# Kernel optimization log

Measured on AMD Instinct MI355X. Metric: run time of the kernel, lower is better.

## Reference

```python
import jax, jax.numpy as jnp
import numpy as np

B, Z, H, D, T, L = 2048, 64, 256, 8, 250, 2


def setup_inputs() -> dict:
    key = jax.random.key(0)
    ks = jax.random.split(key, 10)
    s = 0.05  # small init scale for stable LSTM dynamics
    n = lambda k, shp, sc=1.0: jax.random.normal(k, shp, dtype=jnp.float32) * sc
    return {
        "z": n(ks[0], (B, Z)),
        "target_seq": n(ks[1], (B, T, D)),
        "fc_hidden_w": n(ks[2], (Z, H * L), s),
        "fc_hidden_b": jnp.zeros((H * L,), jnp.float32),
        "fc_cell_w": n(ks[3], (Z, H * L), s),
        "fc_cell_b": jnp.zeros((H * L,), jnp.float32),
        "W_ih0": n(ks[4], (D, 4 * H), s),
        "W_hh0": n(ks[5], (H, 4 * H), s),
        "b_ih0": jnp.zeros((4 * H,), jnp.float32),
        "b_hh0": jnp.zeros((4 * H,), jnp.float32),
        "W_ih1": n(ks[6], (H, 4 * H), s),
        "W_hh1": n(ks[7], (H, 4 * H), s),
        "b_ih1": jnp.zeros((4 * H,), jnp.float32),
        "b_hh1": jnp.zeros((4 * H,), jnp.float32),
        "fc_out_w": n(ks[8], (H, D), s),
        "fc_out_b": jnp.zeros((D,), jnp.float32),
    }


def _lstm_cell(x, h, c, Wih, Whh, bih, bhh):
    # PyTorch gate order: i, f, g, o
    gates = x @ Wih + bih + h @ Whh + bhh  # [B, 4H]
    i, f, g, o = jnp.split(gates, 4, axis=-1)
    c_new = jax.nn.sigmoid(f) * c + jax.nn.sigmoid(i) * jnp.tanh(g)
    h_new = jax.nn.sigmoid(o) * jnp.tanh(c_new)
    return h_new, c_new


def reference(z, target_seq, fc_hidden_w, fc_hidden_b, fc_cell_w, fc_cell_b,
              W_ih0, W_hh0, b_ih0, b_hh0, W_ih1, W_hh1, b_ih1, b_hh1,
              fc_out_w, fc_out_b):
    bsz = z.shape[0]
    # Faithful to torch .view(num_layers, batch, hidden) on [B, H*L] output
    h0_all = (z @ fc_hidden_w + fc_hidden_b).reshape(L, bsz, H)
    c0_all = (z @ fc_cell_w + fc_cell_b).reshape(L, bsz, H)
    # Teacher forcing ratio 1.0: input at step t is target[:, t-1] (zeros at t=0)
    first = jnp.zeros((bsz, 1, target_seq.shape[-1]), target_seq.dtype)
    inputs = jnp.concatenate([first, target_seq[:, :-1]], axis=1)  # [B, T, D]
    xs = jnp.transpose(inputs, (1, 0, 2))  # time-major [T, B, D]

    def step(carry, xt):
        h0, c0, h1, c1 = carry
        h0, c0 = _lstm_cell(xt, h0, c0, W_ih0, W_hh0, b_ih0, b_hh0)
        h1, c1 = _lstm_cell(h0, h1, c1, W_ih1, W_hh1, b_ih1, b_hh1)
        return (h0, c0, h1, c1), h1

    init = (h0_all[0], c0_all[0], h0_all[1], c0_all[1])
    _, hs = jax.lax.scan(step, init, xs)  # hs: [T, B, H]
    hs = jnp.transpose(hs, (1, 0, 2))  # [B, T, H]
    reconstructed = hs @ fc_out_w + fc_out_b  # [B, T, D]
    return reconstructed
```

## Files before the change

### kernel.cpp

```cpp
#include <hip/hip_runtime.h>
#include <cstddef>
#include <cstdint>


#define BSZ    2048
#define ZDIM   64
#define HDIM   256
#define DDIM   8
#define TSTEPS 250
#define ROWS   16
#define NWG    (BSZ / ROWS)
#define NTH    512
#define G4     1024
#define WSTR   264

typedef __attribute__((ext_vector_type(4))) int v4i;

__device__ __forceinline__ unsigned short f2bf(float x) {
  union { float f; unsigned u; } v; v.f = x;
  unsigned r = v.u + 0x7fff + ((v.u >> 16) & 1);
  return (unsigned short)(r >> 16);
}
__device__ __forceinline__ float bf2f(unsigned short b) {
  union { unsigned u; float f; } v; v.u = (unsigned)b << 16; return v.f;
}
__device__ __forceinline__ float fexp2(float x) { return __builtin_amdgcn_exp2f(x); }
__device__ __forceinline__ float frcp(float x)  { return __builtin_amdgcn_rcpf(x); }
__device__ __forceinline__ float sigm(float x)  { return frcp(1.f + fexp2(-1.44269504f * x)); }
__device__ __forceinline__ float tanh_(float x) { return 2.f * frcp(1.f + fexp2(-2.88539008f * x)) - 1.f; }
__device__ __forceinline__ char q8(float x, float s) {
  float v = fminf(fmaxf(x * s, -127.f), 127.f);
  return (char)(int)__builtin_rintf(v);
}
__device__ __forceinline__ void q8pair(float h, float s, char* hi, char* lo) {
  float hs = fminf(fmaxf(h * s, -127.f), 127.f);
  float hq = __builtin_rintf(hs);
  *hi = (char)(int)hq;
  *lo = (char)(int)__builtin_rintf((hs - hq) * 254.f);
}

__global__ void init_state(const float* __restrict__ z,
                           const float* __restrict__ Wfh, const float* __restrict__ bfh,
                           const float* __restrict__ Wfc, const float* __restrict__ bfc,
                           char* __restrict__ h0h, char* __restrict__ h0l,
                           char* __restrict__ h1h, char* __restrict__ h1l,
                           float* __restrict__ c0s, float* __restrict__ c1s)
{
  int idx = blockIdx.x * 256 + threadIdx.x;
  int b = idx >> 8;
  int j = idx & 255;
  int col = ((b & 1) << 8) | j;
  const float* z0 = z + (size_t)(b >> 1) * ZDIM;
  const float* z1 = z + (size_t)(1024 + (b >> 1)) * ZDIM;
  float h0 = bfh[col], c0v = bfc[col], h1 = bfh[col], c1v = bfc[col];
  for (int k = 0; k < ZDIM; ++k) {
    float wh = Wfh[k * 512 + col];
    float wc = Wfc[k * 512 + col];
    float a = z0[k], bb = z1[k];
    h0  += a * wh;  c0v += a * wc;
    h1  += bb * wh; c1v += bb * wc;
  }
  char hi, lo;
  q8pair(h0, 31.75f, &hi, &lo); h0h[idx] = hi; h0l[idx] = lo;
  q8pair(h1, 31.75f, &hi, &lo); h1h[idx] = hi; h1l[idx] = lo;
  c0s[idx] = c0v; c1s[idx] = c1v;
}

__global__ void col_scales(const float* __restrict__ Whh0,
                           const float* __restrict__ Wih1, const float* __restrict__ Whh1,
                           float* __restrict__ cs0, float* __restrict__ qs0,
                           float* __restrict__ cs1, float* __restrict__ qs1)
{
  int c = blockIdx.x * 256 + threadIdx.x;
  if (c < 1024) {
    float m = 0.f;
    for (int k = 0; k < 256; ++k) m = fmaxf(m, fabsf(Whh0[(size_t)k * G4 + c]));
    cs0[c] = m * (1.f / 16129.f);
    qs0[c] = 127.f / m;
  } else {
    c -= 1024;
    float m = 0.f;
    for (int k = 0; k < 256; ++k) m = fmaxf(m, fabsf(Whh1[(size_t)k * G4 + c]));
    for (int k = 0; k < 256; ++k) m = fmaxf(m, fabsf(Wih1[(size_t)k * G4 + c]));
    cs1[c] = m * (1.f / 16129.f);
    qs1[c] = 127.f / m;
  }
}

__global__ void pack_i8(const float* __restrict__ Whh0,
                        const float* __restrict__ Wih1, const float* __restrict__ Whh1,
                        const float* __restrict__ qs0, const float* __restrict__ qs1,
                        char* __restrict__ p0, char* __restrict__ p1)
{
  int tt   = blockIdx.x * 4 + (threadIdx.x >> 6);
  int lane = threadIdx.x & 63;
  int l15 = lane & 15, lq = lane >> 4;
  union { char c[16]; uint4 u; } v;
  if (tt < 256) {
    int w = tt >> 5, kc = (tt >> 3) & 3, i = tt & 7;
    int nt = (i >> 1) * 16 + 2 * w + (i & 1);
    int col = nt * 16 + l15;
    float q = qs0[col];
    for (int j = 0; j < 16; ++j) {
      int k = kc * 64 + lq * 16 + j;
      v.c[j] = q8(Whh0[(size_t)k * G4 + col], q);
    }
    *(uint4*)(p0 + (size_t)tt * 1024 + lane * 16) = v.u;
  } else {
    int t1 = tt - 256;
    int w = t1 >> 6, kc = (t1 >> 3) & 7, i = t1 & 7;
    int nt = (i >> 1) * 16 + 2 * w + (i & 1);
    int col = nt * 16 + l15;
    float q = qs1[col];
    for (int j = 0; j < 16; ++j) {
      int k = kc * 64 + lq * 16 + j;
      float wv = (k < 256) ? Whh1[(size_t)k * G4 + col]
                           : Wih1[(size_t)(k - 256) * G4 + col];
      v.c[j] = q8(wv, q);
    }
    *(uint4*)(p1 + (size_t)t1 * 1024 + lane * 16) = v.u;
  }
}

__global__ __launch_bounds__(NTH, 1) void lstm_run(
    const float* __restrict__ target,
    const char* __restrict__ p0, const char* __restrict__ p1,
    const float* __restrict__ bih0, const float* __restrict__ bhh0,
    const float* __restrict__ bih1, const float* __restrict__ bhh1,
    const float* __restrict__ Wih0,
    const float* __restrict__ Wout, const float* __restrict__ bout,
    const char* __restrict__ h0h, const char* __restrict__ h0l,
    const char* __restrict__ h1h, const char* __restrict__ h1l,
    const float* __restrict__ c0s, const float* __restrict__ c1s,
    const float* __restrict__ cs0, const float* __restrict__ cs1,
    float* __restrict__ out)
{
  __shared__ uint4 X4h[1024];
  __shared__ uint4 X4l[1024];
  __shared__ unsigned short h1f[2][16 * WSTR];
  __shared__ unsigned short woutT[8 * WSTR];

  const int tid  = threadIdx.x;
  const int w    = tid >> 6;
  const int lane = tid & 63;
  const int l15  = lane & 15;
  const int lq   = lane >> 4;
  const int b0   = blockIdx.x * ROWS;
  char* Xch = (char*)X4h;
  char* Xcl = (char*)X4l;

  {
    int m = tid & 15, blk = tid >> 4;
    const char* sh = (blk < 16) ? h1h : h0h;
    const char* sl = (blk < 16) ? h1l : h0l;
    int jblk = blk & 15;
    X4h[blk * 16 + m] = *(const uint4*)(sh + (size_t)(b0 + m) * HDIM + jblk * 16);
    X4l[blk * 16 + m] = *(const uint4*)(sl + (size_t)(b0 + m) * HDIM + jblk * 16);
  }
  for (int i = tid; i < HDIM * DDIM; i += NTH) {
    int k = i >> 3, d = i & 7;
    woutT[d * WSTR + k] = f2bf(Wout[i]);
  }

  const int myrow = lq * 4;
  const int jc0   = 32 * w + l15;
  float c0r[2][4], c1r[2][4];
  float bA0[8], bA1[8], csA0[8], csA1[8];
  float wx[8][8];
#pragma unroll
  for (int i = 0; i < 8; ++i) {
    int col = (i >> 1) * 256 + jc0 + 16 * (i & 1);
    bA0[i]  = bih0[col] + bhh0[col];
    bA1[i]  = bih1[col] + bhh1[col];
    csA0[i] = cs0[col];
    csA1[i] = cs1[col];
#pragma unroll
    for (int d = 0; d < 8; ++d) wx[i][d] = Wih0[d * G4 + col];
  }
#pragma unroll
  for (int cc = 0; cc < 2; ++cc) {
    int j = jc0 + cc * 16;
#pragma unroll
    for (int r = 0; r < 4; ++r) {
      c0r[cc][r] = c0s[(size_t)(b0 + myrow + r) * HDIM + j];
      c1r[cc][r] = c1s[(size_t)(b0 + myrow + r) * HDIM + j];
    }
  }
  const int opr = tid >> 5, opd = (tid >> 2) & 7, opq = tid & 3;
  const float bo_out = bout[opd];

  const char* gp0 = p0 + (size_t)w * 32768 + lane * 16;
  const char* gp1 = p1 + (size_t)w * 65536 + lane * 16;

  v4i breg[8];
#pragma unroll
  for (int s = 0; s < 8; ++s)
    breg[s] = *(const v4i*)(gp0 + (size_t)s * 1024);

  __syncthreads();

#pragma unroll 1
  for (int t = 0; t < TSTEPS; ++t) {
    const int xc = (t & 1) << 9;
    const int xn = xc ^ 512;

    float4 xa[4], xb[4];
    if (t > 0) {
      const float* xp = target + (size_t)(b0 + myrow) * (TSTEPS * DDIM)
                               + (size_t)(t - 1) * DDIM;
#pragma unroll
      for (int r = 0; r < 4; ++r) {
        xa[r] = *(const float4*)(xp + (size_t)r * (TSTEPS * DDIM));
        xb[r] = *(const float4*)(xp + (size_t)r * (TSTEPS * DDIM) + 4);
      }
    } else {
#pragma unroll
      for (int r = 0; r < 4; ++r) {
        xa[r] = make_float4(0.f, 0.f, 0.f, 0.f);
        xb[r] = make_float4(0.f, 0.f, 0.f, 0.f);
      }
    }

    const float sc0 = (t <= 1) ? 4.f : 1.f;
    const float sc1 = (t == 0) ? 4.f : 1.f;
    const float wq0 = (t == 0) ? 31.75f : 127.f;

    v4i acch[8], accl[8];
    const v4i zi = {0, 0, 0, 0};

#pragma unroll
    for (int i = 0; i < 8; ++i) { acch[i] = zi; accl[i] = zi; }
    {
      v4i ah, al;
#pragma unroll 8
      for (int j = 0; j < 32; ++j) {
        const int i = j & 7;
        if (i == 0) {
          int kc = j >> 3;
          int aidx = xc + (16 + kc * 4 + lq) * 16 + l15;
          ah = __builtin_bit_cast(v4i, X4h[aidx]);
          al = __builtin_bit_cast(v4i, X4l[aidx]);
        }
        acch[i] = __builtin_amdgcn_mfma_i32_16x16x64_i8(ah, breg[i], acch[i], 0, 0, 0);
        accl[i] = __builtin_amdgcn_mfma_i32_16x16x64_i8(al, breg[i], accl[i], 0, 0, 0);
        const int jn = j + 8;
        breg[i] = (jn < 32) ? *(const v4i*)(gp0 + (size_t)jn * 1024)
                            : *(const v4i*)(gp1 + (size_t)(jn - 32) * 1024);
      }
    }

    if (t > 0) {
      const unsigned short* hf = h1f[(t & 1) ^ 1];
      float s_ = 0.f;
#pragma unroll
      for (int i = 0; i < 16; ++i) {
        ushort4 hx = *(const ushort4*)&hf[opr * WSTR + i * 16 + opq * 4];
        ushort4 wv = *(const ushort4*)&woutT[opd * WSTR + i * 16 + opq * 4];
        s_ += bf2f(hx.x) * bf2f(wv.x) + bf2f(hx.y) * bf2f(wv.y)
            + bf2f(hx.z) * bf2f(wv.z) + bf2f(hx.w) * bf2f(wv.w);
      }
      s_ += __shfl_xor(s_, 1);
      s_ += __shfl_xor(s_, 2);
      if (opq == 0)
        out[(size_t)(b0 + opr) * (TSTEPS * DDIM) + (size_t)(t - 1) * DDIM + opd] =
            s_ + bo_out;
    }

    {
#pragma unroll
      for (int cc = 0; cc < 2; ++cc) {
        float gf4[4][4];
#pragma unroll
        for (int g = 0; g < 4; ++g) {
          int i = g * 2 + cc;
          float cs = csA0[i] * sc0;
#pragma unroll
          for (int r = 0; r < 4; ++r)
            gf4[g][r] = ((float)acch[i][r] + (float)accl[i][r] * (1.f / 254.f)) * cs + bA0[i];
        }
#pragma unroll
        for (int g = 0; g < 4; ++g) {
          int i = g * 2 + cc;
#pragma unroll
          for (int r = 0; r < 4; ++r)
            gf4[g][r] += xa[r].x * wx[i][0] + xa[r].y * wx[i][1]
                       + xa[r].z * wx[i][2] + xa[r].w * wx[i][3]
                       + xb[r].x * wx[i][4] + xb[r].y * wx[i][5]
                       + xb[r].z * wx[i][6] + xb[r].w * wx[i][7];
        }
#pragma unroll
        for (int r = 0; r < 4; ++r) {
          float iv = sigm(gf4[0][r]);
          float fv = sigm(gf4[1][r]);
          float gv = tanh_(gf4[2][r]);
          float ov = sigm(gf4[3][r]);
          c0r[cc][r] = fv * c0r[cc][r] + iv * gv;
          char hi, lo;
          q8pair(ov * tanh_(c0r[cc][r]), wq0, &hi, &lo);
          int off = (xn + (16 + 2 * w + cc) * 16 + myrow + r) * 16 + l15;
          Xch[off] = hi; Xcl[off] = lo;
        }
      }
    }
    __syncthreads();

#pragma unroll
    for (int i = 0; i < 8; ++i) { acch[i] = zi; accl[i] = zi; }
    {
      v4i ah, al;
#pragma unroll 8
      for (int j = 0; j < 64; ++j) {
        const int i = j & 7;
        if (i == 0) {
          int kc = j >> 3;
          int aidx = (kc < 4) ? (xc + (kc * 4 + lq) * 16 + l15)
                              : (xn + (16 + (kc - 4) * 4 + lq) * 16 + l15);
          ah = __builtin_bit_cast(v4i, X4h[aidx]);
          al = __builtin_bit_cast(v4i, X4l[aidx]);
        }
        acch[i] = __builtin_amdgcn_mfma_i32_16x16x64_i8(ah, breg[i], acch[i], 0, 0, 0);
        accl[i] = __builtin_amdgcn_mfma_i32_16x16x64_i8(al, breg[i], accl[i], 0, 0, 0);
        const int jn = j + 8;
        breg[i] = (jn < 64) ? *(const v4i*)(gp1 + (size_t)jn * 1024)
                            : *(const v4i*)(gp0 + (size_t)(jn - 64) * 1024);
      }
    }

#pragma unroll
    for (int cc = 0; cc < 2; ++cc)
#pragma unroll
      for (int r = 0; r < 4; ++r) {
        float di = ((float)acch[0 + cc][r] + (float)accl[0 + cc][r] * (1.f / 254.f));
        float df = ((float)acch[2 + cc][r] + (float)accl[2 + cc][r] * (1.f / 254.f));
        float dg = ((float)acch[4 + cc][r] + (float)accl[4 + cc][r] * (1.f / 254.f));
        float dv = ((float)acch[6 + cc][r] + (float)accl[6 + cc][r] * (1.f / 254.f));
        float iv = sigm(di * csA1[0 + cc] * sc1 + bA1[0 + cc]);
        float fv = sigm(df * csA1[2 + cc] * sc1 + bA1[2 + cc]);
        float gv = tanh_(dg * csA1[4 + cc] * sc1 + bA1[4 + cc]);
        float ov = sigm(dv * csA1[6 + cc] * sc1 + bA1[6 + cc]);
        c1r[cc][r] = fv * c1r[cc][r] + iv * gv;
        float h = ov * tanh_(c1r[cc][r]);
        char hi, lo;
        q8pair(h, 127.f, &hi, &lo);
        int off = (xn + (2 * w + cc) * 16 + myrow + r) * 16 + l15;
        Xch[off] = hi; Xcl[off] = lo;
        h1f[t & 1][(myrow + r) * WSTR + jc0 + cc * 16] = f2bf(h);
      }
    __syncthreads();
  }

  {
    const unsigned short* hf = h1f[(TSTEPS - 1) & 1];
    float s_ = 0.f;
#pragma unroll
    for (int i = 0; i < 16; ++i) {
      ushort4 hx = *(const ushort4*)&hf[opr * WSTR + i * 16 + opq * 4];
      ushort4 wv = *(const ushort4*)&woutT[opd * WSTR + i * 16 + opq * 4];
      s_ += bf2f(hx.x) * bf2f(wv.x) + bf2f(hx.y) * bf2f(wv.y)
          + bf2f(hx.z) * bf2f(wv.z) + bf2f(hx.w) * bf2f(wv.w);
    }
    s_ += __shfl_xor(s_, 1);
    s_ += __shfl_xor(s_, 2);
    if (opq == 0)
      out[(size_t)(b0 + opr) * (TSTEPS * DDIM) + (size_t)(TSTEPS - 1) * DDIM + opd] =
          s_ + bo_out;
  }
}

extern "C" void kernel_launch(void* const* d_in, const int* in_sizes, int n_in,
                              void* d_out, int out_size, void* d_ws, size_t ws_size,
                              hipStream_t stream) {
  const float* z    = (const float*)d_in[0];
  const float* tgt  = (const float*)d_in[1];
  const float* Wfh  = (const float*)d_in[2];
  const float* bfh  = (const float*)d_in[3];
  const float* Wfc  = (const float*)d_in[4];
  const float* bfc  = (const float*)d_in[5];
  const float* Wih0 = (const float*)d_in[6];
  const float* Whh0 = (const float*)d_in[7];
  const float* bih0 = (const float*)d_in[8];
  const float* bhh0 = (const float*)d_in[9];
  const float* Wih1 = (const float*)d_in[10];
  const float* Whh1 = (const float*)d_in[11];
  const float* bih1 = (const float*)d_in[12];
  const float* bhh1 = (const float*)d_in[13];
  const float* Wout = (const float*)d_in[14];
  const float* bout = (const float*)d_in[15];

  char* ws = (char*)d_ws;
  char*  p0   = ws;
  char*  p1   = ws + 262144;
  char*  h0h  = ws + 786432;
  char*  h0l  = ws + 1310720;
  char*  h1h  = ws + 1835008;
  char*  h1l  = ws + 2359296;
  float* c0s  = (float*)(ws + 2883584);
  float* c1s  = (float*)(ws + 4980736);
  float* cs0  = (float*)(ws + 7077888);
  float* qs0  = (float*)(ws + 7081984);
  float* cs1  = (float*)(ws + 7086080);
  float* qs1  = (float*)(ws + 7090176);

  hipLaunchKernelGGL(init_state, dim3(BSZ * HDIM / 256), dim3(256), 0, stream,
                     z, Wfh, bfh, Wfc, bfc, h0h, h0l, h1h, h1l, c0s, c1s);
  hipLaunchKernelGGL(col_scales, dim3(8), dim3(256), 0, stream,
                     Whh0, Wih1, Whh1, cs0, qs0, cs1, qs1);
  hipLaunchKernelGGL(pack_i8, dim3(192), dim3(256), 0, stream,
                     Whh0, Wih1, Whh1, qs0, qs1, p0, p1);
  hipLaunchKernelGGL(lstm_run, dim3(NWG), dim3(NTH), 0, stream,
                     tgt, p0, p1, bih0, bhh0, bih1, bhh1, Wih0, Wout, bout,
                     h0h, h0l, h1h, h1l, c0s, c1s, cs0, cs1, (float*)d_out);
}
```

Measured before the change: 3.076 ms.

## Double threads per block: each wave owns one 16-column gate slice

Raises the LSTM kernel from 8 to 16 waves per workgroup, with each wave handling one 16-column hidden slice across all four gates instead of two. Weight packing is reordered to match, halving the MFMA count and streamed int8 weight tiles per wave per step. The input-projection weights move from registers into LDS to cut register pressure, and the output projection is spread over 1024 threads. This trades more waves per barrier and extra LDS traffic for more parallelism hiding MFMA and global-load latency in the serial time loop.

```diff
diff --git a/kernel.cpp b/kernel.cpp
--- a/kernel.cpp
+++ b/kernel.cpp
@@ -10,7 +10,7 @@
 #define TSTEPS 250
 #define ROWS   16
 #define NWG    (BSZ / ROWS)
-#define NTH    512
+#define NTH    1024
 #define G4     1024
 #define WSTR   264
 
@@ -97,9 +97,9 @@
   int l15 = lane & 15, lq = lane >> 4;
   union { char c[16]; uint4 u; } v;
   if (tt < 256) {
-    int w = tt >> 5, kc = (tt >> 3) & 3, i = tt & 7;
-    int nt = (i >> 1) * 16 + 2 * w + (i & 1);
-    int col = nt * 16 + l15;
+    int w = tt >> 4, r = tt & 15;
+    int kc = r >> 2, g = r & 3;
+    int col = g * 256 + w * 16 + l15;
     float q = qs0[col];
     for (int j = 0; j < 16; ++j) {
       int k = kc * 64 + lq * 16 + j;
@@ -108,9 +108,9 @@
     *(uint4*)(p0 + (size_t)tt * 1024 + lane * 16) = v.u;
   } else {
     int t1 = tt - 256;
-    int w = t1 >> 6, kc = (t1 >> 3) & 7, i = t1 & 7;
-    int nt = (i >> 1) * 16 + 2 * w + (i & 1);
-    int col = nt * 16 + l15;
+    int w = t1 >> 5, r = t1 & 31;
+    int kc = r >> 2, g = r & 3;
+    int col = g * 256 + w * 16 + l15;
     float q = qs1[col];
     for (int j = 0; j < 16; ++j) {
       int k = kc * 64 + lq * 16 + j;
@@ -122,7 +122,7 @@
   }
 }
 
-__global__ __launch_bounds__(NTH, 1) void lstm_run(
+__global__ __launch_bounds__(NTH, 4) void lstm_run(
     const float* __restrict__ target,
     const char* __restrict__ p0, const char* __restrict__ p1,
     const float* __restrict__ bih0, const float* __restrict__ bhh0,
@@ -139,7 +139,7 @@
   __shared__ uint4 X4l[1024];
   __shared__ unsigned short h1f[2][16 * WSTR];
   __shared__ unsigned short woutT[8 * WSTR];
-
+  __shared__ float wxl[1024 * 8];
   const int tid  = threadIdx.x;
   const int w    = tid >> 6;
   const int lane = tid & 63;
@@ -149,7 +149,7 @@
   char* Xch = (char*)X4h;
   char* Xcl = (char*)X4l;
 
-  {
+  if (tid < 512) {
     int m = tid & 15, blk = tid >> 4;
     const char* sh = (blk < 16) ? h1h : h0h;
     const char* sl = (blk < 16) ? h1l : h0l;
@@ -161,36 +161,34 @@
     int k = i >> 3, d = i & 7;
     woutT[d * WSTR + k] = f2bf(Wout[i]);
   }
+  for (int i = tid; i < G4 * DDIM; i += NTH) {
+    int col = i >> 3, d = i & 7;
+    wxl[i] = Wih0[d * G4 + col];
+  }
 
   const int myrow = lq * 4;
-  const int jc0   = 32 * w + l15;
-  float c0r[2][4], c1r[2][4];
-  float bA0[8], bA1[8], csA0[8], csA1[8];
-  float wx[8][8];
-#pragma unroll
-  for (int i = 0; i < 8; ++i) {
-    int col = (i >> 1) * 256 + jc0 + 16 * (i & 1);
-    bA0[i]  = bih0[col] + bhh0[col];
-    bA1[i]  = bih1[col] + bhh1[col];
-    csA0[i] = cs0[col];
-    csA1[i] = cs1[col];
-#pragma unroll
-    for (int d = 0; d < 8; ++d) wx[i][d] = Wih0[d * G4 + col];
-  }
-#pragma unroll
-  for (int cc = 0; cc < 2; ++cc) {
-    int j = jc0 + cc * 16;
-#pragma unroll
-    for (int r = 0; r < 4; ++r) {
-      c0r[cc][r] = c0s[(size_t)(b0 + myrow + r) * HDIM + j];
-      c1r[cc][r] = c1s[(size_t)(b0 + myrow + r) * HDIM + j];
-    }
-  }
-  const int opr = tid >> 5, opd = (tid >> 2) & 7, opq = tid & 3;
+  const int jc    = 16 * w + l15;
+  float c0r[4], c1r[4];
+  float bA0[4], bA1[4], csA0[4], csA1[4];
+#pragma unroll
+  for (int g = 0; g < 4; ++g) {
+    int col = g * 256 + jc;
+    bA0[g]  = bih0[col] + bhh0[col];
+    bA1[g]  = bih1[col] + bhh1[col];
+    csA0[g] = cs0[col];
+    csA1[g] = cs1[col];
+  }
+#pragma unroll
+  for (int r = 0; r < 4; ++r) {
+    c0r[r] = c0s[(size_t)(b0 + myrow + r) * HDIM + jc];
+    c1r[r] = c1s[(size_t)(b0 + myrow + r) * HDIM + jc];
+  }
+  const int oidx = tid >> 3, opq = tid & 7;
+  const int opr = oidx >> 3, opd = oidx & 7;
   const float bo_out = bout[opd];
 
-  const char* gp0 = p0 + (size_t)w * 32768 + lane * 16;
-  const char* gp1 = p1 + (size_t)w * 65536 + lane * 16;
+  const char* gp0 = p0 + (size_t)w * 16384 + lane * 16;
+  const char* gp1 = p1 + (size_t)w * 32768 + lane * 16;
 
   v4i breg[8];
 #pragma unroll
@@ -225,127 +223,118 @@
     const float sc1 = (t == 0) ? 4.f : 1.f;
     const float wq0 = (t == 0) ? 31.75f : 127.f;
 
-    v4i acch[8], accl[8];
+    v4i acch[4], accl[4];
     const v4i zi = {0, 0, 0, 0};
 
 #pragma unroll
-    for (int i = 0; i < 8; ++i) { acch[i] = zi; accl[i] = zi; }
+    for (int g = 0; g < 4; ++g) { acch[g] = zi; accl[g] = zi; }
+    {
+      v4i ah, al;
+#pragma unroll 8
+      for (int j = 0; j < 16; ++j) {
+        const int g = j & 3, s = j & 7;
+        if (g == 0) {
+          int kc = j >> 2;
+          int aidx = xc + (16 + kc * 4 + lq) * 16 + l15;
+          ah = __builtin_bit_cast(v4i, X4h[aidx]);
+          al = __builtin_bit_cast(v4i, X4l[aidx]);
+        }
+        acch[g] = __builtin_amdgcn_mfma_i32_16x16x64_i8(ah, breg[s], acch[g], 0, 0, 0);
+        accl[g] = __builtin_amdgcn_mfma_i32_16x16x64_i8(al, breg[s], accl[g], 0, 0, 0);
+        const int jn = j + 8;
+        breg[s] = (jn < 16) ? *(const v4i*)(gp0 + (size_t)jn * 1024)
+                            : *(const v4i*)(gp1 + (size_t)(jn - 16) * 1024);
+      }
+    }
+
+    if (t > 0) {
+      const unsigned short* hf = h1f[(t & 1) ^ 1];
+      float s_ = 0.f;
+#pragma unroll
+      for (int i = 0; i < 8; ++i) {
+        ushort4 hx = *(const ushort4*)&hf[opr * WSTR + i * 32 + opq * 4];
+        ushort4 wv = *(const ushort4*)&woutT[opd * WSTR + i * 32 + opq * 4];
+        s_ += bf2f(hx.x) * bf2f(wv.x) + bf2f(hx.y) * bf2f(wv.y)
+            + bf2f(hx.z) * bf2f(wv.z) + bf2f(hx.w) * bf2f(wv.w);
+      }
+      s_ += __shfl_xor(s_, 1);
+      s_ += __shfl_xor(s_, 2);
+      s_ += __shfl_xor(s_, 4);
+      if (opq == 0)
+        out[(size_t)(b0 + opr) * (TSTEPS * DDIM) + (size_t)(t - 1) * DDIM + opd] =
+            s_ + bo_out;
+    }
+
+    {
+      float gf[4][4];
+#pragma unroll
+      for (int g = 0; g < 4; ++g) {
+        float4 wa = *(const float4*)&wxl[(g * 256 + jc) * 8];
+        float4 wb = *(const float4*)&wxl[(g * 256 + jc) * 8 + 4];
+        float cs = csA0[g] * sc0;
+#pragma unroll
+        for (int r = 0; r < 4; ++r) {
+          float d_ = ((float)acch[g][r] + (float)accl[g][r] * (1.f / 254.f)) * cs + bA0[g];
+          gf[g][r] = d_
+              + xa[r].x * wa.x + xa[r].y * wa.y + xa[r].z * wa.z + xa[r].w * wa.w
+              + xb[r].x * wb.x + xb[r].y * wb.y + xb[r].z * wb.z + xb[r].w * wb.w;
+        }
+      }
+#pragma unroll
+      for (int r = 0; r < 4; ++r) {
+        float iv = sigm(gf[0][r]);
+        float fv = sigm(gf[1][r]);
+        float gv = tanh_(gf[2][r]);
+        float ov = sigm(gf[3][r]);
+        c0r[r] = fv * c0r[r] + iv * gv;
+        char hi, lo;
+        q8pair(ov * tanh_(c0r[r]), wq0, &hi, &lo);
+        int off = (xn + (16 + w) * 16 + myrow + r) * 16 + l15;
+        Xch[off] = hi; Xcl[off] = lo;
+      }
+    }
+    __syncthreads();
+
+#pragma unroll
+    for (int g = 0; g < 4; ++g) { acch[g] = zi; accl[g] = zi; }
     {
       v4i ah, al;
 #pragma unroll 8
       for (int j = 0; j < 32; ++j) {
-        const int i = j & 7;
-        if (i == 0) {
-          int kc = j >> 3;
-          int aidx = xc + (16 + kc * 4 + lq) * 16 + l15;
-          ah = __builtin_bit_cast(v4i, X4h[aidx]);
-          al = __builtin_bit_cast(v4i, X4l[aidx]);
-        }
-        acch[i] = __builtin_amdgcn_mfma_i32_16x16x64_i8(ah, breg[i], acch[i], 0, 0, 0);
-        accl[i] = __builtin_amdgcn_mfma_i32_16x16x64_i8(al, breg[i], accl[i], 0, 0, 0);
-        const int jn = j + 8;
-        breg[i] = (jn < 32) ? *(const v4i*)(gp0 + (size_t)jn * 1024)
-                            : *(const v4i*)(gp1 + (size_t)(jn - 32) * 1024);
-      }
-    }
-
-    if (t > 0) {
-      const unsigned short* hf = h1f[(t & 1) ^ 1];
-      float s_ = 0.f;
-#pragma unroll
-      for (int i = 0; i < 16; ++i) {
-        ushort4 hx = *(const ushort4*)&hf[opr * WSTR + i * 16 + opq * 4];
-        ushort4 wv = *(const ushort4*)&woutT[opd * WSTR + i * 16 + opq * 4];
-        s_ += bf2f(hx.x) * bf2f(wv.x) + bf2f(hx.y) * bf2f(wv.y)
-            + bf2f(hx.z) * bf2f(wv.z) + bf2f(hx.w) * bf2f(wv.w);
-      }
-      s_ += __shfl_xor(s_, 1);
-      s_ += __shfl_xor(s_, 2);
-      if (opq == 0)
-        out[(size_t)(b0 + opr) * (TSTEPS * DDIM) + (size_t)(t - 1) * DDIM + opd] =
-            s_ + bo_out;
-    }
-
-    {
-#pragma unroll
-      for (int cc = 0; cc < 2; ++cc) {
-        float gf4[4][4];
-#pragma unroll
-        for (int g = 0; g < 4; ++g) {
-          int i = g * 2 + cc;
-          float cs = csA0[i] * sc0;
-#pragma unroll
-          for (int r = 0; r < 4; ++r)
-            gf4[g][r] = ((float)acch[i][r] + (float)accl[i][r] * (1.f / 254.f)) * cs + bA0[i];
-        }
-#pragma unroll
-        for (int g = 0; g < 4; ++g) {
-          int i = g * 2 + cc;
-#pragma unroll
-          for (int r = 0; r < 4; ++r)
-            gf4[g][r] += xa[r].x * wx[i][0] + xa[r].y * wx[i][1]
-                       + xa[r].z * wx[i][2] + xa[r].w * wx[i][3]
-                       + xb[r].x * wx[i][4] + xb[r].y * wx[i][5]
-                       + xb[r].z * wx[i][6] + xb[r].w * wx[i][7];
-        }
-#pragma unroll
-        for (int r = 0; r < 4; ++r) {
-          float iv = sigm(gf4[0][r]);
-          float fv = sigm(gf4[1][r]);
-          float gv = tanh_(gf4[2][r]);
-          float ov = sigm(gf4[3][r]);
-          c0r[cc][r] = fv * c0r[cc][r] + iv * gv;
-          char hi, lo;
-          q8pair(ov * tanh_(c0r[cc][r]), wq0, &hi, &lo);
-          int off = (xn + (16 + 2 * w + cc) * 16 + myrow + r) * 16 + l15;
-          Xch[off] = hi; Xcl[off] = lo;
-        }
-      }
-    }
-    __syncthreads();
-
-#pragma unroll
-    for (int i = 0; i < 8; ++i) { acch[i] = zi; accl[i] = zi; }
-    {
-      v4i ah, al;
-#pragma unroll 8
-      for (int j = 0; j < 64; ++j) {
-        const int i = j & 7;
-        if (i == 0) {
-          int kc = j >> 3;
+        const int g = j & 3, s = j & 7;
+        if (g == 0) {
+          int kc = j >> 2;
           int aidx = (kc < 4) ? (xc + (kc * 4 + lq) * 16 + l15)
                               : (xn + (16 + (kc - 4) * 4 + lq) * 16 + l15);
           ah = __builtin_bit_cast(v4i, X4h[aidx]);
           al = __builtin_bit_cast(v4i, X4l[aidx]);
         }
-        acch[i] = __builtin_amdgcn_mfma_i32_16x16x64_i8(ah, breg[i], acch[i], 0, 0, 0);
-        accl[i] = __builtin_amdgcn_mfma_i32_16x16x64_i8(al, breg[i], accl[i], 0, 0, 0);
+        acch[g] = __builtin_amdgcn_mfma_i32_16x16x64_i8(ah, breg[s], acch[g], 0, 0, 0);
+        accl[g] = __builtin_amdgcn_mfma_i32_16x16x64_i8(al, breg[s], accl[g], 0, 0, 0);
         const int jn = j + 8;
-        breg[i] = (jn < 64) ? *(const v4i*)(gp1 + (size_t)jn * 1024)
-                            : *(const v4i*)(gp0 + (size_t)(jn - 64) * 1024);
-      }
-    }
-
-#pragma unroll
-    for (int cc = 0; cc < 2; ++cc)
-#pragma unroll
-      for (int r = 0; r < 4; ++r) {
-        float di = ((float)acch[0 + cc][r] + (float)accl[0 + cc][r] * (1.f / 254.f));
-        float df = ((float)acch[2 + cc][r] + (float)accl[2 + cc][r] * (1.f / 254.f));
-        float dg = ((float)acch[4 + cc][r] + (float)accl[4 + cc][r] * (1.f / 254.f));
-        float dv = ((float)acch[6 + cc][r] + (float)accl[6 + cc][r] * (1.f / 254.f));
-        float iv = sigm(di * csA1[0 + cc] * sc1 + bA1[0 + cc]);
-        float fv = sigm(df * csA1[2 + cc] * sc1 + bA1[2 + cc]);
-        float gv = tanh_(dg * csA1[4 + cc] * sc1 + bA1[4 + cc]);
-        float ov = sigm(dv * csA1[6 + cc] * sc1 + bA1[6 + cc]);
-        c1r[cc][r] = fv * c1r[cc][r] + iv * gv;
-        float h = ov * tanh_(c1r[cc][r]);
-        char hi, lo;
-        q8pair(h, 127.f, &hi, &lo);
-        int off = (xn + (2 * w + cc) * 16 + myrow + r) * 16 + l15;
-        Xch[off] = hi; Xcl[off] = lo;
-        h1f[t & 1][(myrow + r) * WSTR + jc0 + cc * 16] = f2bf(h);
-      }
+        breg[s] = (jn < 32) ? *(const v4i*)(gp1 + (size_t)jn * 1024)
+                            : *(const v4i*)(gp0 + (size_t)(jn - 32) * 1024);
+      }
+    }
+
+#pragma unroll
+    for (int r = 0; r < 4; ++r) {
+      float di = ((float)acch[0][r] + (float)accl[0][r] * (1.f / 254.f));
+      float df = ((float)acch[1][r] + (float)accl[1][r] * (1.f / 254.f));
+      float dg = ((float)acch[2][r] + (float)accl[2][r] * (1.f / 254.f));
+      float dv = ((float)acch[3][r] + (float)accl[3][r] * (1.f / 254.f));
+      float iv = sigm(di * csA1[0] * sc1 + bA1[0]);
+      float fv = sigm(df * csA1[1] * sc1 + bA1[1]);
+      float gv = tanh_(dg * csA1[2] * sc1 + bA1[2]);
+      float ov = sigm(dv * csA1[3] * sc1 + bA1[3]);
+      c1r[r] = fv * c1r[r] + iv * gv;
+      float h = ov * tanh_(c1r[r]);
+      char hi, lo;
+      q8pair(h, 127.f, &hi, &lo);
+      int off = (xn + w * 16 + myrow + r) * 16 + l15;
+      Xch[off] = hi; Xcl[off] = lo;
+      h1f[t & 1][(myrow + r) * WSTR + jc] = f2bf(h);
+    }
     __syncthreads();
   }
 
@@ -353,14 +342,15 @@
     const unsigned short* hf = h1f[(TSTEPS - 1) & 1];
     float s_ = 0.f;
 #pragma unroll
-    for (int i = 0; i < 16; ++i) {
-      ushort4 hx = *(const ushort4*)&hf[opr * WSTR + i * 16 + opq * 4];
-      ushort4 wv = *(const ushort4*)&woutT[opd * WSTR + i * 16 + opq * 4];
+    for (int i = 0; i < 8; ++i) {
+      ushort4 hx = *(const ushort4*)&hf[opr * WSTR + i * 32 + opq * 4];
+      ushort4 wv = *(const ushort4*)&woutT[opd * WSTR + i * 32 + opq * 4];
       s_ += bf2f(hx.x) * bf2f(wv.x) + bf2f(hx.y) * bf2f(wv.y)
           + bf2f(hx.z) * bf2f(wv.z) + bf2f(hx.w) * bf2f(wv.w);
     }
     s_ += __shfl_xor(s_, 1);
     s_ += __shfl_xor(s_, 2);
+    s_ += __shfl_xor(s_, 4);
     if (opq == 0)
       out[(size_t)(b0 + opr) * (TSTEPS * DDIM) + (size_t)(TSTEPS - 1) * DDIM + opd] =
           s_ + bo_out;
```

Result: slower. 4.097 ms (+33.2%).

## Split gate MFMAs into two halves and overlap activation math with second half

Applied to the files above, without the earlier changes.

Reorders the packed int8 weight tiles so each wave computes the gates for column chunk cc=0 first and cc=1 second, each half in its own accumulator set. Dequantisation and the LSTM activations for the first half are interleaved into the MFMA loop of the second half, and the output projection is folded into the first layer-0 MFMA loop. The aim is to hide VALU transcendental work and the output projection behind matrix-core latency. Wih0 moves from registers into LDS as float4 tables, freeing registers at the cost of extra LDS reads. The h1f double buffer becomes a single buffer, relying on the existing barrier ordering.

```diff
diff --git a/kernel.cpp b/kernel.cpp
--- a/kernel.cpp
+++ b/kernel.cpp
@@ -97,9 +97,9 @@
   int l15 = lane & 15, lq = lane >> 4;
   union { char c[16]; uint4 u; } v;
   if (tt < 256) {
-    int w = tt >> 5, kc = (tt >> 3) & 3, i = tt & 7;
-    int nt = (i >> 1) * 16 + 2 * w + (i & 1);
-    int col = nt * 16 + l15;
+    int w = tt >> 5, r = tt & 31;
+    int cc = r >> 4, kc = (r >> 2) & 3, g = r & 3;
+    int col = g * 256 + w * 32 + cc * 16 + l15;
     float q = qs0[col];
     for (int j = 0; j < 16; ++j) {
       int k = kc * 64 + lq * 16 + j;
@@ -108,9 +108,9 @@
     *(uint4*)(p0 + (size_t)tt * 1024 + lane * 16) = v.u;
   } else {
     int t1 = tt - 256;
-    int w = t1 >> 6, kc = (t1 >> 3) & 7, i = t1 & 7;
-    int nt = (i >> 1) * 16 + 2 * w + (i & 1);
-    int col = nt * 16 + l15;
+    int w = t1 >> 6, r = t1 & 63;
+    int cc = r >> 5, kc = (r >> 2) & 7, g = r & 3;
+    int col = g * 256 + w * 32 + cc * 16 + l15;
     float q = qs1[col];
     for (int j = 0; j < 16; ++j) {
       int k = kc * 64 + lq * 16 + j;
@@ -137,9 +137,10 @@
 {
   __shared__ uint4 X4h[1024];
   __shared__ uint4 X4l[1024];
-  __shared__ unsigned short h1f[2][16 * WSTR];
+  __shared__ unsigned short h1f[16 * WSTR];
   __shared__ unsigned short woutT[8 * WSTR];
-
+  __shared__ float4 wxa4[1024];
+  __shared__ float4 wxb4[1024];
   const int tid  = threadIdx.x;
   const int w    = tid >> 6;
   const int lane = tid & 63;
@@ -161,12 +162,17 @@
     int k = i >> 3, d = i & 7;
     woutT[d * WSTR + k] = f2bf(Wout[i]);
   }
+  for (int i = tid; i < G4; i += NTH) {
+    wxa4[i] = make_float4(Wih0[0 * G4 + i], Wih0[1 * G4 + i],
+                          Wih0[2 * G4 + i], Wih0[3 * G4 + i]);
+    wxb4[i] = make_float4(Wih0[4 * G4 + i], Wih0[5 * G4 + i],
+                          Wih0[6 * G4 + i], Wih0[7 * G4 + i]);
+  }
 
   const int myrow = lq * 4;
   const int jc0   = 32 * w + l15;
   float c0r[2][4], c1r[2][4];
   float bA0[8], bA1[8], csA0[8], csA1[8];
-  float wx[8][8];
 #pragma unroll
   for (int i = 0; i < 8; ++i) {
     int col = (i >> 1) * 256 + jc0 + 16 * (i & 1);
@@ -174,8 +180,6 @@
     bA1[i]  = bih1[col] + bhh1[col];
     csA0[i] = cs0[col];
     csA1[i] = cs1[col];
-#pragma unroll
-    for (int d = 0; d < 8; ++d) wx[i][d] = Wih0[d * G4 + col];
   }
 #pragma unroll
   for (int cc = 0; cc < 2; ++cc) {
@@ -225,136 +229,173 @@
     const float sc1 = (t == 0) ? 4.f : 1.f;
     const float wq0 = (t == 0) ? 31.75f : 127.f;
 
-    v4i acch[8], accl[8];
+    v4i pAh[4], pAl[4], pBh[4], pBl[4];
     const v4i zi = {0, 0, 0, 0};
-
-#pragma unroll
-    for (int i = 0; i < 8; ++i) { acch[i] = zi; accl[i] = zi; }
+    float gf0[4][4];
+
+    auto DEQ0 = [&](const v4i* ph, const v4i* pl, int cc, int g, float (*gf)[4]) {
+      int i = g * 2 + cc;
+      int col = g * 256 + jc0 + cc * 16;
+      float4 wa = wxa4[col];
+      float4 wb = wxb4[col];
+      float cs = csA0[i] * sc0;
+#pragma unroll
+      for (int r = 0; r < 4; ++r)
+        gf[g][r] = ((float)ph[g][r] + (float)pl[g][r] * (1.f / 254.f)) * cs + bA0[i]
+            + xa[r].x * wa.x + xa[r].y * wa.y + xa[r].z * wa.z + xa[r].w * wa.w
+            + xb[r].x * wb.x + xb[r].y * wb.y + xb[r].z * wb.z + xb[r].w * wb.w;
+    };
+    auto ACT0 = [&](int cc, int r, float (*gf)[4]) {
+      float iv = sigm(gf[0][r]);
+      float fv = sigm(gf[1][r]);
+      float gv = tanh_(gf[2][r]);
+      float ov = sigm(gf[3][r]);
+      c0r[cc][r] = fv * c0r[cc][r] + iv * gv;
+      char hi, lo;
+      q8pair(ov * tanh_(c0r[cc][r]), wq0, &hi, &lo);
+      int off = (xn + (16 + 2 * w + cc) * 16 + myrow + r) * 16 + l15;
+      Xch[off] = hi; Xcl[off] = lo;
+    };
+    auto CELL1R = [&](const v4i* ph, const v4i* pl, int cc, int r) {
+      float di = ((float)ph[0][r] + (float)pl[0][r] * (1.f / 254.f)) * csA1[0 + cc] * sc1 + bA1[0 + cc];
+      float df = ((float)ph[1][r] + (float)pl[1][r] * (1.f / 254.f)) * csA1[2 + cc] * sc1 + bA1[2 + cc];
+      float dg = ((float)ph[2][r] + (float)pl[2][r] * (1.f / 254.f)) * csA1[4 + cc] * sc1 + bA1[4 + cc];
+      float dv = ((float)ph[3][r] + (float)pl[3][r] * (1.f / 254.f)) * csA1[6 + cc] * sc1 + bA1[6 + cc];
+      float iv = sigm(di);
+      float fv = sigm(df);
+      float gv = tanh_(dg);
+      float ov = sigm(dv);
+      c1r[cc][r] = fv * c1r[cc][r] + iv * gv;
+      float h = ov * tanh_(c1r[cc][r]);
+      char hi, lo;
+      q8pair(h, 127.f, &hi, &lo);
+      int off = (xn + (2 * w + cc) * 16 + myrow + r) * 16 + l15;
+      Xch[off] = hi; Xcl[off] = lo;
+      h1f[(myrow + r) * WSTR + jc0 + cc * 16] = f2bf(h);
+    };
+
+#pragma unroll
+    for (int g = 0; g < 4; ++g) { pAh[g] = zi; pAl[g] = zi; }
+    {
+      v4i ah, al;
+      float os_ = 0.f;
+#pragma unroll
+      for (int j = 0; j < 16; ++j) {
+        const int g = j & 3, s = j & 7;
+        if (g == 0) {
+          int kc = j >> 2;
+          int aidx = xc + (16 + kc * 4 + lq) * 16 + l15;
+          ah = __builtin_bit_cast(v4i, X4h[aidx]);
+          al = __builtin_bit_cast(v4i, X4l[aidx]);
+        }
+        pAh[g] = __builtin_amdgcn_mfma_i32_16x16x64_i8(ah, breg[s], pAh[g], 0, 0, 0);
+        pAl[g] = __builtin_amdgcn_mfma_i32_16x16x64_i8(al, breg[s], pAl[g], 0, 0, 0);
+        if (t > 0) {
+          ushort4 hx = *(const ushort4*)&h1f[opr * WSTR + j * 16 + opq * 4];
+          ushort4 wv = *(const ushort4*)&woutT[opd * WSTR + j * 16 + opq * 4];
+          os_ += bf2f(hx.x) * bf2f(wv.x) + bf2f(hx.y) * bf2f(wv.y)
+               + bf2f(hx.z) * bf2f(wv.z) + bf2f(hx.w) * bf2f(wv.w);
+        }
+        const int jn = j + 8;
+        breg[s] = *(const v4i*)(gp0 + (size_t)jn * 1024);
+      }
+      if (t > 0) {
+        os_ += __shfl_xor(os_, 1);
+        os_ += __shfl_xor(os_, 2);
+        if (opq == 0)
+          out[(size_t)(b0 + opr) * (TSTEPS * DDIM) + (size_t)(t - 1) * DDIM + opd] =
+              os_ + bo_out;
+      }
+    }
+
+#pragma unroll
+    for (int g = 0; g < 4; ++g) { pBh[g] = zi; pBl[g] = zi; }
+    {
+      v4i ah, al;
+#pragma unroll
+      for (int j = 0; j < 16; ++j) {
+        const int g = j & 3, s = j & 7;
+        if (g == 0) {
+          int kc = j >> 2;
+          int aidx = xc + (16 + kc * 4 + lq) * 16 + l15;
+          ah = __builtin_bit_cast(v4i, X4h[aidx]);
+          al = __builtin_bit_cast(v4i, X4l[aidx]);
+        }
+        pBh[g] = __builtin_amdgcn_mfma_i32_16x16x64_i8(ah, breg[s], pBh[g], 0, 0, 0);
+        pBl[g] = __builtin_amdgcn_mfma_i32_16x16x64_i8(al, breg[s], pBl[g], 0, 0, 0);
+        if (j & 1) {
+          const int p = j >> 1;
+          if (p < 4) DEQ0(pAh, pAl, 0, p, gf0);
+          else       ACT0(0, p - 4, gf0);
+        }
+        const int jn = j + 24;
+        breg[s] = (jn < 32) ? *(const v4i*)(gp0 + (size_t)jn * 1024)
+                            : *(const v4i*)(gp1 + (size_t)(jn - 32) * 1024);
+      }
+    }
+    {
+      float gf1[4][4];
+#pragma unroll
+      for (int g = 0; g < 4; ++g) DEQ0(pBh, pBl, 1, g, gf1);
+#pragma unroll
+      for (int r = 0; r < 4; ++r) ACT0(1, r, gf1);
+    }
+    __syncthreads();
+
+#pragma unroll
+    for (int g = 0; g < 4; ++g) { pAh[g] = zi; pAl[g] = zi; }
     {
       v4i ah, al;
 #pragma unroll 8
       for (int j = 0; j < 32; ++j) {
-        const int i = j & 7;
-        if (i == 0) {
-          int kc = j >> 3;
-          int aidx = xc + (16 + kc * 4 + lq) * 16 + l15;
-          ah = __builtin_bit_cast(v4i, X4h[aidx]);
-          al = __builtin_bit_cast(v4i, X4l[aidx]);
-        }
-        acch[i] = __builtin_amdgcn_mfma_i32_16x16x64_i8(ah, breg[i], acch[i], 0, 0, 0);
-        accl[i] = __builtin_amdgcn_mfma_i32_16x16x64_i8(al, breg[i], accl[i], 0, 0, 0);
-        const int jn = j + 8;
-        breg[i] = (jn < 32) ? *(const v4i*)(gp0 + (size_t)jn * 1024)
-                            : *(const v4i*)(gp1 + (size_t)(jn - 32) * 1024);
-      }
-    }
-
-    if (t > 0) {
-      const unsigned short* hf = h1f[(t & 1) ^ 1];
-      float s_ = 0.f;
-#pragma unroll
-      for (int i = 0; i < 16; ++i) {
-        ushort4 hx = *(const ushort4*)&hf[opr * WSTR + i * 16 + opq * 4];
-        ushort4 wv = *(const ushort4*)&woutT[opd * WSTR + i * 16 + opq * 4];
-        s_ += bf2f(hx.x) * bf2f(wv.x) + bf2f(hx.y) * bf2f(wv.y)
-            + bf2f(hx.z) * bf2f(wv.z) + bf2f(hx.w) * bf2f(wv.w);
-      }
-      s_ += __shfl_xor(s_, 1);
-      s_ += __shfl_xor(s_, 2);
-      if (opq == 0)
-        out[(size_t)(b0 + opr) * (TSTEPS * DDIM) + (size_t)(t - 1) * DDIM + opd] =
-            s_ + bo_out;
-    }
-
-    {
-#pragma unroll
-      for (int cc = 0; cc < 2; ++cc) {
-        float gf4[4][4];
-#pragma unroll
-        for (int g = 0; g < 4; ++g) {
-          int i = g * 2 + cc;
-          float cs = csA0[i] * sc0;
-#pragma unroll
-          for (int r = 0; r < 4; ++r)
-            gf4[g][r] = ((float)acch[i][r] + (float)accl[i][r] * (1.f / 254.f)) * cs + bA0[i];
-        }
-#pragma unroll
-        for (int g = 0; g < 4; ++g) {
-          int i = g * 2 + cc;
-#pragma unroll
-          for (int r = 0; r < 4; ++r)
-            gf4[g][r] += xa[r].x * wx[i][0] + xa[r].y * wx[i][1]
-                       + xa[r].z * wx[i][2] + xa[r].w * wx[i][3]
-                       + xb[r].x * wx[i][4] + xb[r].y * wx[i][5]
-                       + xb[r].z * wx[i][6] + xb[r].w * wx[i][7];
-        }
-#pragma unroll
-        for (int r = 0; r < 4; ++r) {
-          float iv = sigm(gf4[0][r]);
-          float fv = sigm(gf4[1][r]);
-          float gv = tanh_(gf4[2][r]);
-          float ov = sigm(gf4[3][r]);
-          c0r[cc][r] = fv * c0r[cc][r] + iv * gv;
-          char hi, lo;
-          q8pair(ov * tanh_(c0r[cc][r]), wq0, &hi, &lo);
-          int off = (xn + (16 + 2 * w + cc) * 16 + myrow + r) * 16 + l15;
-          Xch[off] = hi; Xcl[off] = lo;
-        }
-      }
-    }
-    __syncthreads();
-
-#pragma unroll
-    for (int i = 0; i < 8; ++i) { acch[i] = zi; accl[i] = zi; }
-    {
-      v4i ah, al;
-#pragma unroll 8
-      for (int j = 0; j < 64; ++j) {
-        const int i = j & 7;
-        if (i == 0) {
-          int kc = j >> 3;
+        const int g = j & 3, s = j & 7;
+        if (g == 0) {
+          int kc = j >> 2;
           int aidx = (kc < 4) ? (xc + (kc * 4 + lq) * 16 + l15)
                               : (xn + (16 + (kc - 4) * 4 + lq) * 16 + l15);
           ah = __builtin_bit_cast(v4i, X4h[aidx]);
           al = __builtin_bit_cast(v4i, X4l[aidx]);
         }
-        acch[i] = __builtin_amdgcn_mfma_i32_16x16x64_i8(ah, breg[i], acch[i], 0, 0, 0);
-        accl[i] = __builtin_amdgcn_mfma_i32_16x16x64_i8(al, breg[i], accl[i], 0, 0, 0);
+        pAh[g] = __builtin_amdgcn_mfma_i32_16x16x64_i8(ah, breg[s], pAh[g], 0, 0, 0);
+        pAl[g] = __builtin_amdgcn_mfma_i32_16x16x64_i8(al, breg[s], pAl[g], 0, 0, 0);
         const int jn = j + 8;
-        breg[i] = (jn < 64) ? *(const v4i*)(gp1 + (size_t)jn * 1024)
+        breg[s] = *(const v4i*)(gp1 + (size_t)jn * 1024);
+      }
+    }
+
+#pragma unroll
+    for (int g = 0; g < 4; ++g) { pBh[g] = zi; pBl[g] = zi; }
+    {
+      v4i ah, al;
+#pragma unroll
+      for (int j = 0; j < 32; ++j) {
+        const int g = j & 3, s = j & 7;
+        if (g == 0) {
+          int kc = j >> 2;
+          int aidx = (kc < 4) ? (xc + (kc * 4 + lq) * 16 + l15)
+                              : (xn + (16 + (kc - 4) * 4 + lq) * 16 + l15);
+          ah = __builtin_bit_cast(v4i, X4h[aidx]);
+          al = __builtin_bit_cast(v4i, X4l[aidx]);
+        }
+        pBh[g] = __builtin_amdgcn_mfma_i32_16x16x64_i8(ah, breg[s], pBh[g], 0, 0, 0);
+        pBl[g] = __builtin_amdgcn_mfma_i32_16x16x64_i8(al, breg[s], pBl[g], 0, 0, 0);
+        if ((j & 7) == 1) CELL1R(pAh, pAl, 0, j >> 3);
+        const int jn = j + 40;
+        breg[s] = (jn < 64) ? *(const v4i*)(gp1 + (size_t)jn * 1024)
                             : *(const v4i*)(gp0 + (size_t)(jn - 64) * 1024);
       }
     }
-
-#pragma unroll
-    for (int cc = 0; cc < 2; ++cc)
-#pragma unroll
-      for (int r = 0; r < 4; ++r) {
-        float di = ((float)acch[0 + cc][r] + (float)accl[0 + cc][r] * (1.f / 254.f));
-        float df = ((float)acch[2 + cc][r] + (float)accl[2 + cc][r] * (1.f / 254.f));
-        float dg = ((float)acch[4 + cc][r] + (float)accl[4 + cc][r] * (1.f / 254.f));
-        float dv = ((float)acch[6 + cc][r] + (float)accl[6 + cc][r] * (1.f / 254.f));
-        float iv = sigm(di * csA1[0 + cc] * sc1 + bA1[0 + cc]);
-        float fv = sigm(df * csA1[2 + cc] * sc1 + bA1[2 + cc]);
-        float gv = tanh_(dg * csA1[4 + cc] * sc1 + bA1[4 + cc]);
-        float ov = sigm(dv * csA1[6 + cc] * sc1 + bA1[6 + cc]);
-        c1r[cc][r] = fv * c1r[cc][r] + iv * gv;
-        float h = ov * tanh_(c1r[cc][r]);
-        char hi, lo;
-        q8pair(h, 127.f, &hi, &lo);
-        int off = (xn + (2 * w + cc) * 16 + myrow + r) * 16 + l15;
-        Xch[off] = hi; Xcl[off] = lo;
-        h1f[t & 1][(myrow + r) * WSTR + jc0 + cc * 16] = f2bf(h);
-      }
+#pragma unroll
+    for (int r = 0; r < 4; ++r) CELL1R(pBh, pBl, 1, r);
+
     __syncthreads();
   }
 
   {
-    const unsigned short* hf = h1f[(TSTEPS - 1) & 1];
     float s_ = 0.f;
 #pragma unroll
     for (int i = 0; i < 16; ++i) {
-      ushort4 hx = *(const ushort4*)&hf[opr * WSTR + i * 16 + opq * 4];
+      ushort4 hx = *(const ushort4*)&h1f[opr * WSTR + i * 16 + opq * 4];
       ushort4 wv = *(const ushort4*)&woutT[opd * WSTR + i * 16 + opq * 4];
       s_ += bf2f(hx.x) * bf2f(wv.x) + bf2f(hx.y) * bf2f(wv.y)
           + bf2f(hx.z) * bf2f(wv.z) + bf2f(hx.w) * bf2f(wv.w);
```

Measured after the change: 5.669 ms. 84.3% more time.

## Keep first layer-0 weight slices and Wih0 in LDS to cut register pressure

Applied to the files above, without the earlier changes.

Each wave now stages the first eight slices of its int8 layer-0 recurrent weights in shared memory and streams only the remaining slices from global memory through the register ring. The layer-0 step reads those first slices from LDS, and the wrap-around prefetch at the end of the layer-1 loop now starts at slice 8. The 64 per-thread input-projection weights (wx) move into LDS as float4 pairs and are loaded per gate inside the fused gate computation. The aim is to cut global weight traffic per step and free registers, at the cost of roughly 160KB of LDS and extra LDS reads per step.

```diff
diff --git a/kernel.cpp b/kernel.cpp
--- a/kernel.cpp
+++ b/kernel.cpp
@@ -139,7 +139,9 @@
   __shared__ uint4 X4l[1024];
   __shared__ unsigned short h1f[2][16 * WSTR];
   __shared__ unsigned short woutT[8 * WSTR];
-
+  __shared__ float4 wxa4[1024];
+  __shared__ float4 wxb4[1024];
+  __shared__ uint4 wres[8 * 8 * 64];
   const int tid  = threadIdx.x;
   const int w    = tid >> 6;
   const int lane = tid & 63;
@@ -161,12 +163,17 @@
     int k = i >> 3, d = i & 7;
     woutT[d * WSTR + k] = f2bf(Wout[i]);
   }
+  for (int i = tid; i < G4; i += NTH) {
+    wxa4[i] = make_float4(Wih0[0 * G4 + i], Wih0[1 * G4 + i],
+                          Wih0[2 * G4 + i], Wih0[3 * G4 + i]);
+    wxb4[i] = make_float4(Wih0[4 * G4 + i], Wih0[5 * G4 + i],
+                          Wih0[6 * G4 + i], Wih0[7 * G4 + i]);
+  }
 
   const int myrow = lq * 4;
   const int jc0   = 32 * w + l15;
   float c0r[2][4], c1r[2][4];
   float bA0[8], bA1[8], csA0[8], csA1[8];
-  float wx[8][8];
 #pragma unroll
   for (int i = 0; i < 8; ++i) {
     int col = (i >> 1) * 256 + jc0 + 16 * (i & 1);
@@ -174,8 +181,6 @@
     bA1[i]  = bih1[col] + bhh1[col];
     csA0[i] = cs0[col];
     csA1[i] = cs1[col];
-#pragma unroll
-    for (int d = 0; d < 8; ++d) wx[i][d] = Wih0[d * G4 + col];
   }
 #pragma unroll
   for (int cc = 0; cc < 2; ++cc) {
@@ -192,10 +197,14 @@
   const char* gp0 = p0 + (size_t)w * 32768 + lane * 16;
   const char* gp1 = p1 + (size_t)w * 65536 + lane * 16;
 
+#pragma unroll
+  for (int j = 0; j < 8; ++j)
+    wres[w * 512 + j * 64 + lane] = *(const uint4*)(gp0 + (size_t)j * 1024);
+
   v4i breg[8];
 #pragma unroll
   for (int s = 0; s < 8; ++s)
-    breg[s] = *(const v4i*)(gp0 + (size_t)s * 1024);
+    breg[s] = *(const v4i*)(gp0 + (size_t)(8 + s) * 1024);
 
   __syncthreads();
 
@@ -232,19 +241,37 @@
     for (int i = 0; i < 8; ++i) { acch[i] = zi; accl[i] = zi; }
     {
       v4i ah, al;
+      {
+        int aidx = xc + (16 + lq) * 16 + l15;
+        ah = __builtin_bit_cast(v4i, X4h[aidx]);
+        al = __builtin_bit_cast(v4i, X4l[aidx]);
+      }
+      {
+        v4i rb[2];
+        rb[0] = __builtin_bit_cast(v4i, wres[w * 512 + lane]);
+#pragma unroll
+        for (int j = 0; j < 8; ++j) {
+          if (j < 7)
+            rb[(j + 1) & 1] = __builtin_bit_cast(v4i, wres[w * 512 + (j + 1) * 64 + lane]);
+          v4i bb = rb[j & 1];
+          acch[j] = __builtin_amdgcn_mfma_i32_16x16x64_i8(ah, bb, acch[j], 0, 0, 0);
+          accl[j] = __builtin_amdgcn_mfma_i32_16x16x64_i8(al, bb, accl[j], 0, 0, 0);
+        }
+      }
 #pragma unroll 8
-      for (int j = 0; j < 32; ++j) {
-        const int i = j & 7;
+      for (int j = 8; j < 32; ++j) {
+        const int i = j & 7, s = j & 7;
         if (i == 0) {
           int kc = j >> 3;
           int aidx = xc + (16 + kc * 4 + lq) * 16 + l15;
           ah = __builtin_bit_cast(v4i, X4h[aidx]);
           al = __builtin_bit_cast(v4i, X4l[aidx]);
         }
-        acch[i] = __builtin_amdgcn_mfma_i32_16x16x64_i8(ah, breg[i], acch[i], 0, 0, 0);
-        accl[i] = __builtin_amdgcn_mfma_i32_16x16x64_i8(al, breg[i], accl[i], 0, 0, 0);
+        v4i bb = breg[s];
+        acch[i] = __builtin_amdgcn_mfma_i32_16x16x64_i8(ah, bb, acch[i], 0, 0, 0);
+        accl[i] = __builtin_amdgcn_mfma_i32_16x16x64_i8(al, bb, accl[i], 0, 0, 0);
         const int jn = j + 8;
-        breg[i] = (jn < 32) ? *(const v4i*)(gp0 + (size_t)jn * 1024)
+        breg[s] = (jn < 32) ? *(const v4i*)(gp0 + (size_t)jn * 1024)
                             : *(const v4i*)(gp1 + (size_t)(jn - 32) * 1024);
       }
     }
@@ -273,20 +300,15 @@
 #pragma unroll
         for (int g = 0; g < 4; ++g) {
           int i = g * 2 + cc;
+          int col = g * 256 + jc0 + cc * 16;
+          float4 wa = wxa4[col];
+          float4 wb = wxb4[col];
           float cs = csA0[i] * sc0;
 #pragma unroll
           for (int r = 0; r < 4; ++r)
-            gf4[g][r] = ((float)acch[i][r] + (float)accl[i][r] * (1.f / 254.f)) * cs + bA0[i];
-        }
-#pragma unroll
-        for (int g = 0; g < 4; ++g) {
-          int i = g * 2 + cc;
-#pragma unroll
-          for (int r = 0; r < 4; ++r)
-            gf4[g][r] += xa[r].x * wx[i][0] + xa[r].y * wx[i][1]
-                       + xa[r].z * wx[i][2] + xa[r].w * wx[i][3]
-                       + xb[r].x * wx[i][4] + xb[r].y * wx[i][5]
-                       + xb[r].z * wx[i][6] + xb[r].w * wx[i][7];
+            gf4[g][r] = ((float)acch[i][r] + (float)accl[i][r] * (1.f / 254.f)) * cs + bA0[i]
+                + xa[r].x * wa.x + xa[r].y * wa.y + xa[r].z * wa.z + xa[r].w * wa.w
+                + xb[r].x * wb.x + xb[r].y * wb.y + xb[r].z * wb.z + xb[r].w * wb.w;
         }
 #pragma unroll
         for (int r = 0; r < 4; ++r) {
@@ -322,7 +344,7 @@
         accl[i] = __builtin_amdgcn_mfma_i32_16x16x64_i8(al, breg[i], accl[i], 0, 0, 0);
         const int jn = j + 8;
         breg[i] = (jn < 64) ? *(const v4i*)(gp1 + (size_t)jn * 1024)
-                            : *(const v4i*)(gp0 + (size_t)(jn - 64) * 1024);
+                            : *(const v4i*)(gp0 + (size_t)(jn - 64 + 8) * 1024);
       }
     }
 
```

New measurement: 2.762 ms. -10.2%, faster.
